# Kernel optimization log

Measured on AMD Instinct MI355X. Metric: run time of the kernel, lower is better.

## Reference

```python
import jax, jax.numpy as jnp
import numpy as np

N_SRC = 100000
N_DST = 100000
E = 500000
D = 128
L = 2


def _sage(x_src, x_dst, e_src, e_dst, W_self, W_neigh, b):
    # DGL SAGEConv('mean'): out = x_dst @ W_self^T + mean_neighbors(x_src) @ W_neigh^T + b
    n_dst = x_dst.shape[0]
    msg_sum = jax.ops.segment_sum(x_src[e_src], e_dst, num_segments=n_dst)  # [n_dst, D]
    deg = jax.ops.segment_sum(jnp.ones((e_dst.shape[0],), x_src.dtype), e_dst, num_segments=n_dst)
    h_neigh = msg_sum / jnp.maximum(deg, 1.0)[:, None]  # isolated nodes -> 0
    return x_dst @ W_self.T + h_neigh @ W_neigh.T + b


def setup_inputs() -> dict:
    key = jax.random.key(0)
    ks = jax.random.split(key, 10)
    s = 1.0 / np.sqrt(D)
    return {
        "x_src": jax.random.normal(ks[0], (N_SRC, D), jnp.float32),
        "x_dst": jax.random.normal(ks[1], (N_DST, D), jnp.float32),
        "e_src": jax.random.randint(ks[2], (E,), 0, N_SRC, jnp.int32),
        "e_dst": jax.random.randint(ks[3], (E,), 0, N_DST, jnp.int32),
        "W_ship_self": jax.random.normal(ks[4], (L, D, D), jnp.float32) * s,
        "W_ship_neigh": jax.random.normal(ks[5], (L, D, D), jnp.float32) * s,
        "b_ship": jnp.zeros((L, D), jnp.float32),
        "W_rev_self": jax.random.normal(ks[6], (L, D, D), jnp.float32) * s,
        "W_rev_neigh": jax.random.normal(ks[7], (L, D, D), jnp.float32) * s,
        "b_rev": jnp.zeros((L, D), jnp.float32),
    }


def reference(x_src, x_dst, e_src, e_dst, W_ship_self, W_ship_neigh, b_ship,
              W_rev_self, W_rev_neigh, b_rev):
    h_s, h_d = x_src, x_dst
    n_layers = W_ship_self.shape[0]
    for l in range(n_layers):
        # ('source','ship','destination'): messages source -> destination
        new_d = _sage(h_s, h_d, e_src, e_dst, W_ship_self[l], W_ship_neigh[l], b_ship[l])
        # ('destination','rev_ship','source'): messages destination -> source
        new_s = _sage(h_d, h_s, e_dst, e_src, W_rev_self[l], W_rev_neigh[l], b_rev[l])
        h_d = jax.nn.relu(new_d)
        h_s = jax.nn.relu(new_s)
        # dropout p=0.0 (eval) -> identity
    return h_s, h_d
```

## Files before the change

### kernel.cpp

```cpp
#include <hip/hip_runtime.h>
#include <hip/hip_bf16.h>

#define NN 100000
#define EDGES 500000
#define DD 128
#define NBKT 196
#define SLACK 3584
#define CHUNK 4096
#define BPD ((EDGES + CHUNK - 1) / CHUNK)

typedef short bf16x8 __attribute__((ext_vector_type(8)));
typedef float f32x4  __attribute__((ext_vector_type(4)));

__device__ __forceinline__ unsigned short f2bf(float f) {
    unsigned u = __float_as_uint(f);
    u += 0x7fffu + ((u >> 16) & 1u);
    return (unsigned short)(u >> 16);
}

__global__ void f2bx_kernel(const float* __restrict__ a, const float* __restrict__ b,
                            unsigned short* __restrict__ oa, unsigned short* __restrict__ ob) {
    const float* in = blockIdx.y ? b : a;
    unsigned short* out = blockIdx.y ? ob : oa;
    int i = blockIdx.x * 256 + threadIdx.x;
    float4 v = ((const float4*)in)[i];
    ushort4 o;
    o.x = f2bf(v.x); o.y = f2bf(v.y); o.z = f2bf(v.z); o.w = f2bf(v.w);
    ((ushort4*)out)[i] = o;
}

__global__ void f2bw_kernel(const float* __restrict__ w0, const float* __restrict__ w1,
                            const float* __restrict__ w2, const float* __restrict__ w3,
                            unsigned short* __restrict__ o0, unsigned short* __restrict__ o1,
                            unsigned short* __restrict__ o2, unsigned short* __restrict__ o3) {
    const float* in; unsigned short* out;
    switch (blockIdx.y) {
        case 0: in = w0; out = o0; break;
        case 1: in = w1; out = o1; break;
        case 2: in = w2; out = o2; break;
        default: in = w3; out = o3; break;
    }
    int i = blockIdx.x * 256 + threadIdx.x;
    float4 v = ((const float4*)in)[i];
    ushort4 o;
    o.x = f2bf(v.x); o.y = f2bf(v.y); o.z = f2bf(v.z); o.w = f2bf(v.w);
    ((ushort4*)out)[i] = o;
}

__global__ __launch_bounds__(256) void bin_scatter_kernel(
    const int* __restrict__ e_src, const int* __restrict__ e_dst,
    int* __restrict__ gcnt,
    unsigned* __restrict__ recbin)
{
    const int dir = blockIdx.y;
    const int t = threadIdx.x;
    const int c0 = blockIdx.x * CHUNK;
    const int nvalid = min(CHUNK, EDGES - c0);
    const int* __restrict__ TGT = dir ? e_src : e_dst;
    const int* __restrict__ PAY = dir ? e_dst : e_src;

    __shared__ int hist[256];
    __shared__ int lbase[256];
    __shared__ int lofs[256];
    __shared__ int scanA[256], scanB[256];
    __shared__ int laddr[CHUNK];
    __shared__ unsigned lrec[CHUNK];

    hist[t] = 0;
    __syncthreads();

    int myb[16], myslot[16];
    unsigned myrec[16];
    #pragma unroll
    for (int j = 0; j < 16; ++j) {
        int e = c0 + j * 256 + t;
        myb[j] = -1;
        if (e < EDGES) {
            int tgt = TGT[e], pay = PAY[e];
            int b = tgt >> 9;
            myb[j] = b;
            myrec[j] = ((unsigned)pay << 9) | (unsigned)(tgt & 511);
            myslot[j] = atomicAdd(&hist[b], 1);
        }
    }
    __syncthreads();
    int cnt = hist[t];
    lbase[t] = (cnt > 0) ? atomicAdd(&gcnt[dir * 256 + t], cnt) : 0;
    scanA[t] = cnt;
    __syncthreads();
    int* pa = scanA; int* pb = scanB;
    for (int d = 1; d < 256; d <<= 1) {
        pb[t] = pa[t] + (t >= d ? pa[t - d] : 0);
        __syncthreads();
        int* tmp = pa; pa = pb; pb = tmp;
    }
    lofs[t] = pa[t] - cnt;
    __syncthreads();
    #pragma unroll
    for (int j = 0; j < 16; ++j) {
        if (myb[j] >= 0) {
            int b = myb[j];
            int pos = lofs[b] + myslot[j];
            int g = lbase[b] + myslot[j];
            lrec[pos] = myrec[j];
            laddr[pos] = (g < SLACK) ? (b * SLACK + g) : -1;
        }
    }
    __syncthreads();
    unsigned* __restrict__ out = recbin + (size_t)dir * NBKT * SLACK;
    #pragma unroll
    for (int j = 0; j < 16; ++j) {
        int i = j * 256 + t;
        if (i < nvalid) {
            int a = laddr[i];
            if (a >= 0) out[a] = lrec[i];
        }
    }
}

__global__ void bucket_scan_kernel(const int* __restrict__ gcnt, int* __restrict__ csr_base) {
    int t = threadIdx.x;
    __shared__ int A[256], B[256];
    for (int dir = 0; dir < 2; ++dir) {
        int c = (t < NBKT) ? min(gcnt[dir * 256 + t], SLACK) : 0;
        A[t] = c;
        __syncthreads();
        int* pa = A; int* pb = B;
        for (int d = 1; d < 256; d <<= 1) {
            pb[t] = pa[t] + (t >= d ? pa[t - d] : 0);
            __syncthreads();
            int* tmp = pa; pa = pb; pb = tmp;
        }
        if (t < NBKT) csr_base[dir * 200 + t] = pa[t] - c;
        if (t == 0)   csr_base[dir * 200 + NBKT] = pa[255];
        __syncthreads();
    }
}

__global__ __launch_bounds__(256) void fine_place_kernel(
    const unsigned* __restrict__ recbin, const int* __restrict__ gcnt,
    const int* __restrict__ csr_base,
    int* __restrict__ rp_dst, int* __restrict__ rp_src,
    float* __restrict__ inv_dst, float* __restrict__ inv_src,
    int* __restrict__ csr_dst, int* __restrict__ csr_src)
{
    const int dir = blockIdx.y;
    const int bkt = blockIdx.x;
    const int t = threadIdx.x;
    int*   __restrict__ rp  = dir ? rp_src  : rp_dst;
    float* __restrict__ inv = dir ? inv_src : inv_dst;
    int*   __restrict__ csr = dir ? csr_src : csr_dst;
    const unsigned* __restrict__ recs = recbin + ((size_t)dir * NBKT + bkt) * SLACK;
    const int cnt = min(gcnt[dir * 256 + bkt], SLACK);
    const int cbase = csr_base[dir * 200 + bkt];
    const int n0 = bkt * 512;

    __shared__ int deg[512];
    __shared__ int sA[512], sB[512];
    __shared__ int cur[512];
    deg[t] = 0; deg[t + 256] = 0;
    __syncthreads();
    for (int i = t; i < cnt; i += 256)
        atomicAdd(&deg[recs[i] & 511u], 1);
    __syncthreads();
    sA[t] = deg[t]; sA[t + 256] = deg[t + 256];
    __syncthreads();
    int* pa = sA; int* pb = sB;
    for (int d = 1; d < 512; d <<= 1) {
        pb[t]       = pa[t]       + (t >= d           ? pa[t - d]       : 0);
        pb[t + 256] = pa[t + 256] + ((t + 256) >= d   ? pa[t + 256 - d] : 0);
        __syncthreads();
        int* tmp = pa; pa = pb; pb = tmp;
    }
    #pragma unroll
    for (int k = 0; k < 2; ++k) {
        int i = t + k * 256;
        int off = pa[i] - deg[i];
        cur[i] = off;
        int node = n0 + i;
        if (node < NN) {
            rp[node] = cbase + off;
            inv[node] = 1.0f / (float)max(deg[i], 1);
        }
    }
    if (bkt == NBKT - 1 && t == 0) rp[NN] = csr_base[dir * 200 + NBKT];
    __syncthreads();
    for (int i = t; i < cnt; i += 256) {
        unsigned r = recs[i];
        int p = atomicAdd(&cur[r & 511u], 1);
        csr[cbase + p] = (int)(r >> 9);
    }
}

__global__ void aggregate2_kernel(
    const unsigned short* __restrict__ h0, const int* __restrict__ rp0,
    const int* __restrict__ csr0, const float* __restrict__ inv0, unsigned short* __restrict__ ag0,
    const unsigned short* __restrict__ h1, const int* __restrict__ rp1,
    const int* __restrict__ csr1, const float* __restrict__ inv1, unsigned short* __restrict__ ag1)
{
    const int dir = blockIdx.y;
    const unsigned short* __restrict__ h = dir ? h1 : h0;
    const int* __restrict__ rp   = dir ? rp1 : rp0;
    const int* __restrict__ csr  = dir ? csr1 : csr0;
    const float* __restrict__ inv = dir ? inv1 : inv0;
    unsigned short* __restrict__ agg = dir ? ag1 : ag0;

    int wid  = (int)((blockIdx.x * 256u + threadIdx.x) >> 6);
    int lane = threadIdx.x & 63;
    if (wid >= NN) return;
    int beg = rp[wid], end = rp[wid + 1];
    float s0 = 0.f, s1 = 0.f, t0 = 0.f, t1 = 0.f;
    float u0 = 0.f, u1 = 0.f, v0 = 0.f, v1 = 0.f;
    int i = beg;
    for (; i + 3 < end; i += 4) {
        int c0 = csr[i], c1 = csr[i + 1], c2 = csr[i + 2], c3 = csr[i + 3];
        unsigned w0 = *(const unsigned*)(h + (size_t)c0 * DD + lane * 2);
        unsigned w1 = *(const unsigned*)(h + (size_t)c1 * DD + lane * 2);
        unsigned w2 = *(const unsigned*)(h + (size_t)c2 * DD + lane * 2);
        unsigned w3 = *(const unsigned*)(h + (size_t)c3 * DD + lane * 2);
        s0 += __uint_as_float(w0 << 16); s1 += __uint_as_float(w0 & 0xffff0000u);
        t0 += __uint_as_float(w1 << 16); t1 += __uint_as_float(w1 & 0xffff0000u);
        u0 += __uint_as_float(w2 << 16); u1 += __uint_as_float(w2 & 0xffff0000u);
        v0 += __uint_as_float(w3 << 16); v1 += __uint_as_float(w3 & 0xffff0000u);
    }
    for (; i < end; ++i) {
        unsigned w = *(const unsigned*)(h + (size_t)csr[i] * DD + lane * 2);
        s0 += __uint_as_float(w << 16); s1 += __uint_as_float(w & 0xffff0000u);
    }
    float sc = inv[wid];
    float a0 = ((s0 + t0) + (u0 + v0)) * sc;
    float a1 = ((s1 + t1) + (u1 + v1)) * sc;
    unsigned o = (unsigned)f2bf(a0) | ((unsigned)f2bf(a1) << 16);
    *(unsigned*)(agg + (size_t)wid * DD + lane * 2) = o;
}

__global__ __launch_bounds__(512, 4) void mfma_gemm5_kernel(
    const unsigned short* __restrict__ Hs0, const unsigned short* __restrict__ Ha0,
    const unsigned short* __restrict__ Ws0, const unsigned short* __restrict__ Wn0,
    const float* __restrict__ bias0, float* __restrict__ outF0, unsigned short* __restrict__ outB0,
    const unsigned short* __restrict__ Hs1, const unsigned short* __restrict__ Ha1,
    const unsigned short* __restrict__ Ws1, const unsigned short* __restrict__ Wn1,
    const float* __restrict__ bias1, float* __restrict__ outF1, unsigned short* __restrict__ outB1,
    int M)
{
    const int dir = blockIdx.y;
    const unsigned short* __restrict__ Hself = dir ? Hs1 : Hs0;
    const unsigned short* __restrict__ Hagg  = dir ? Ha1 : Ha0;
    const unsigned short* __restrict__ Wself = dir ? Ws1 : Ws0;
    const unsigned short* __restrict__ Wneigh= dir ? Wn1 : Wn0;
    const float* __restrict__ bias = dir ? bias1 : bias0;
    float* __restrict__ outF = dir ? outF1 : outF0;
    unsigned short* __restrict__ outB = dir ? outB1 : outB0;

    __shared__ __align__(16) unsigned short sW[128 * 256];
    const int tid  = threadIdx.x;
    const int lane = tid & 63;
    const int w    = tid >> 6;
    const int row0 = blockIdx.x * 256;

    #pragma unroll
    for (int i = 0; i < 8; ++i) {
        int q = i * 512 + tid;
        int n = q >> 5, c = q & 31;
        const unsigned short* src = (c < 16) ? (Wself + n * 128 + c * 8)
                                             : (Wneigh + n * 128 + (c - 16) * 8);
        int d = n * 256 + (c & 24) * 8 + (((c ^ n) & 7) * 8);
        *(uint4*)(sW + d) = *(const uint4*)src;
    }

    f32x4 acc[4][4];
    #pragma unroll
    for (int mt = 0; mt < 4; ++mt)
        #pragma unroll
        for (int nt = 0; nt < 4; ++nt) acc[mt][nt] = (f32x4){0.f, 0.f, 0.f, 0.f};

    const int mbase = (w >> 1) * 64;
    const int nbase = (w & 1) * 64;
    const int l15 = lane & 15;
    const int l4  = lane >> 4;

    int voff[4];
    #pragma unroll
    for (int mt = 0; mt < 4; ++mt) {
        int grow = row0 + mbase + mt * 16 + l15;
        if (grow >= M) grow = M - 1;
        voff[mt] = grow * 128 + l4 * 8;
    }

    __syncthreads();

    bf16x8 a_cur[4], a_nxt[4];
    #pragma unroll
    for (int mt = 0; mt < 4; ++mt) a_cur[mt] = *(const bf16x8*)(Hself + voff[mt]);

    #pragma unroll
    for (int ks = 0; ks < 8; ++ks) {
        if (ks < 7) {
            const int ks1 = ks + 1;
            const int col = (ks1 & 3) * 32;
            const unsigned short* __restrict__ base = (ks1 < 4) ? Hself : Hagg;
            #pragma unroll
            for (int mt = 0; mt < 4; ++mt)
                a_nxt[mt] = *(const bf16x8*)(base + voff[mt] + col);
        }
        const int c = ks * 4 + l4;
        #pragma unroll
        for (int mt = 0; mt < 4; ++mt) {
            int n0 = nbase + 0 * 16 + l15;
            int n1 = nbase + 1 * 16 + l15;
            int n2 = nbase + 2 * 16 + l15;
            int n3 = nbase + 3 * 16 + l15;
            bf16x8 b0 = *(const bf16x8*)(sW + n0 * 256 + (c & 24) * 8 + (((c ^ n0) & 7) * 8));
            bf16x8 b1 = *(const bf16x8*)(sW + n1 * 256 + (c & 24) * 8 + (((c ^ n1) & 7) * 8));
            bf16x8 b2 = *(const bf16x8*)(sW + n2 * 256 + (c & 24) * 8 + (((c ^ n2) & 7) * 8));
            bf16x8 b3 = *(const bf16x8*)(sW + n3 * 256 + (c & 24) * 8 + (((c ^ n3) & 7) * 8));
            acc[mt][0] = __builtin_amdgcn_mfma_f32_16x16x32_bf16(a_cur[mt], b0, acc[mt][0], 0, 0, 0);
            acc[mt][1] = __builtin_amdgcn_mfma_f32_16x16x32_bf16(a_cur[mt], b1, acc[mt][1], 0, 0, 0);
            acc[mt][2] = __builtin_amdgcn_mfma_f32_16x16x32_bf16(a_cur[mt], b2, acc[mt][2], 0, 0, 0);
            acc[mt][3] = __builtin_amdgcn_mfma_f32_16x16x32_bf16(a_cur[mt], b3, acc[mt][3], 0, 0, 0);
        }
        #pragma unroll
        for (int mt = 0; mt < 4; ++mt) a_cur[mt] = a_nxt[mt];
    }

    __syncthreads();

    #pragma unroll
    for (int nt = 0; nt < 4; ++nt) {
        int col = nbase + nt * 16 + l15;
        float bj = bias[col];
        #pragma unroll
        for (int mt = 0; mt < 4; ++mt) {
            #pragma unroll
            for (int r = 0; r < 4; ++r) {
                int grow = row0 + mbase + mt * 16 + l4 * 4 + r;
                if (grow < M) {
                    float v = fmaxf(acc[mt][nt][r] + bj, 0.f);
                    if (outF) outF[(size_t)grow * 128 + col] = v;
                    else      outB[(size_t)grow * 128 + col] = f2bf(v);
                }
            }
        }
    }
}

extern "C" void kernel_launch(void* const* d_in, const int* in_sizes, int n_in,
                              void* d_out, int out_size, void* d_ws, size_t ws_size,
                              hipStream_t stream) {
    const float* x_src        = (const float*)d_in[0];
    const float* x_dst        = (const float*)d_in[1];
    const int*   e_src        = (const int*)d_in[2];
    const int*   e_dst        = (const int*)d_in[3];
    const float* W_ship_self  = (const float*)d_in[4];
    const float* W_ship_neigh = (const float*)d_in[5];
    const float* b_ship       = (const float*)d_in[6];
    const float* W_rev_self   = (const float*)d_in[7];
    const float* W_rev_neigh  = (const float*)d_in[8];
    const float* b_rev        = (const float*)d_in[9];
    float* out = (float*)d_out;

    char* ws = (char*)d_ws;
    size_t off = 0;
    auto alloc = [&](size_t bytes) {
        char* p = ws + off;
        off = (off + bytes + 255) & ~(size_t)255;
        return p;
    };
    unsigned short* xs_bf = (unsigned short*)alloc((size_t)NN * DD * 2);
    unsigned short* xd_bf = (unsigned short*)alloc((size_t)NN * DD * 2);
    unsigned short* agg1  = (unsigned short*)alloc((size_t)NN * DD * 2);
    unsigned short* agg2  = (unsigned short*)alloc((size_t)NN * DD * 2);
    unsigned short* Wss_bf = (unsigned short*)alloc(2 * DD * DD * 2);
    unsigned short* Wsn_bf = (unsigned short*)alloc(2 * DD * DD * 2);
    unsigned short* Wrs_bf = (unsigned short*)alloc(2 * DD * DD * 2);
    unsigned short* Wrn_bf = (unsigned short*)alloc(2 * DD * DD * 2);
    int* gcnt = (int*)alloc(2 * 256 * 4);
    int* csr_base = (int*)alloc(2 * 200 * 4);
    unsigned* recbin = (unsigned*)alloc((size_t)2 * NBKT * SLACK * 4);
    int* rp_dst = (int*)alloc((NN + 1) * 4);
    int* rp_src = (int*)alloc((NN + 1) * 4);
    float* inv_dst = (float*)alloc(NN * 4);
    float* inv_src = (float*)alloc(NN * 4);
    int* csr_dst = (int*)alloc(EDGES * 4);
    int* csr_src = (int*)alloc(EDGES * 4);
    (void)ws_size; (void)in_sizes; (void)n_in; (void)out_size;

    hipMemsetAsync(gcnt, 0, 2 * 256 * 4, stream);

    const int xn4 = NN * DD / 4;
    f2bx_kernel<<<dim3(xn4 / 256, 2), 256, 0, stream>>>(x_src, x_dst, xs_bf, xd_bf);
    f2bw_kernel<<<dim3(32, 4), 256, 0, stream>>>(W_ship_self, W_ship_neigh, W_rev_self, W_rev_neigh,
                                                 Wss_bf, Wsn_bf, Wrs_bf, Wrn_bf);

    bin_scatter_kernel<<<dim3(BPD, 2), 256, 0, stream>>>(e_src, e_dst, gcnt, recbin);
    bucket_scan_kernel<<<1, 256, 0, stream>>>(gcnt, csr_base);
    fine_place_kernel<<<dim3(NBKT, 2), 256, 0, stream>>>(recbin, gcnt, csr_base,
        rp_dst, rp_src, inv_dst, inv_src, csr_dst, csr_src);

    float* out_s = out;
    float* out_d = out + (size_t)NN * DD;
    const int gemm_grid = (NN + 255) / 256;
    const int agg_grid  = (NN * 64 + 255) / 256;

    for (int l = 0; l < 2; ++l) {
        aggregate2_kernel<<<dim3(agg_grid, 2), 256, 0, stream>>>(
            xs_bf, rp_dst, csr_dst, inv_dst, agg1,
            xd_bf, rp_src, csr_src, inv_src, agg2);
        mfma_gemm5_kernel<<<dim3(gemm_grid, 2), 512, 0, stream>>>(
            xd_bf, agg1, Wss_bf + l * DD * DD, Wsn_bf + l * DD * DD, b_ship + l * DD,
            l ? out_d : nullptr, l ? nullptr : xd_bf,
            xs_bf, agg2, Wrs_bf + l * DD * DD, Wrn_bf + l * DD * DD, b_rev + l * DD,
            l ? out_s : nullptr, l ? nullptr : xs_bf,
            NN);
    }
}
```

Before: 484.5 us.

## Aggregate with 16 lanes per node using 16-byte loads and batched edge prefetch

The neighbor-mean aggregation now assigns 16 threads per destination node instead of a full 64-lane wavefront. Each thread loads 8 bf16 values with one 16-byte load, and up to 8 edges are prefetched before accumulation. The inverse degree is computed from the row pointers rather than loaded from the inv array. This is meant to cut idle lanes and raise memory-level parallelism on the random gathers, at the cost of more registers and some lane divergence for high-degree nodes.

```diff
diff --git a/kernel.cpp b/kernel.cpp
--- a/kernel.cpp
+++ b/kernel.cpp
@@ -11,6 +11,7 @@
 
 typedef short bf16x8 __attribute__((ext_vector_type(8)));
 typedef float f32x4  __attribute__((ext_vector_type(4)));
+typedef float f32x2  __attribute__((ext_vector_type(2)));
 
 __device__ __forceinline__ unsigned short f2bf(float f) {
     unsigned u = __float_as_uint(f);
@@ -192,46 +193,72 @@
     }
 }
 
-__global__ void aggregate2_kernel(
+__global__ __launch_bounds__(256) void aggregate3_kernel(
     const unsigned short* __restrict__ h0, const int* __restrict__ rp0,
-    const int* __restrict__ csr0, const float* __restrict__ inv0, unsigned short* __restrict__ ag0,
+    const int* __restrict__ csr0, unsigned short* __restrict__ ag0,
     const unsigned short* __restrict__ h1, const int* __restrict__ rp1,
-    const int* __restrict__ csr1, const float* __restrict__ inv1, unsigned short* __restrict__ ag1)
+    const int* __restrict__ csr1, unsigned short* __restrict__ ag1)
 {
     const int dir = blockIdx.y;
     const unsigned short* __restrict__ h = dir ? h1 : h0;
     const int* __restrict__ rp   = dir ? rp1 : rp0;
     const int* __restrict__ csr  = dir ? csr1 : csr0;
-    const float* __restrict__ inv = dir ? inv1 : inv0;
     unsigned short* __restrict__ agg = dir ? ag1 : ag0;
 
-    int wid  = (int)((blockIdx.x * 256u + threadIdx.x) >> 6);
-    int lane = threadIdx.x & 63;
-    if (wid >= NN) return;
-    int beg = rp[wid], end = rp[wid + 1];
-    float s0 = 0.f, s1 = 0.f, t0 = 0.f, t1 = 0.f;
-    float u0 = 0.f, u1 = 0.f, v0 = 0.f, v1 = 0.f;
-    int i = beg;
-    for (; i + 3 < end; i += 4) {
-        int c0 = csr[i], c1 = csr[i + 1], c2 = csr[i + 2], c3 = csr[i + 3];
-        unsigned w0 = *(const unsigned*)(h + (size_t)c0 * DD + lane * 2);
-        unsigned w1 = *(const unsigned*)(h + (size_t)c1 * DD + lane * 2);
-        unsigned w2 = *(const unsigned*)(h + (size_t)c2 * DD + lane * 2);
-        unsigned w3 = *(const unsigned*)(h + (size_t)c3 * DD + lane * 2);
-        s0 += __uint_as_float(w0 << 16); s1 += __uint_as_float(w0 & 0xffff0000u);
-        t0 += __uint_as_float(w1 << 16); t1 += __uint_as_float(w1 & 0xffff0000u);
-        u0 += __uint_as_float(w2 << 16); u1 += __uint_as_float(w2 & 0xffff0000u);
-        v0 += __uint_as_float(w3 << 16); v1 += __uint_as_float(w3 & 0xffff0000u);
-    }
-    for (; i < end; ++i) {
-        unsigned w = *(const unsigned*)(h + (size_t)csr[i] * DD + lane * 2);
-        s0 += __uint_as_float(w << 16); s1 += __uint_as_float(w & 0xffff0000u);
-    }
-    float sc = inv[wid];
-    float a0 = ((s0 + t0) + (u0 + v0)) * sc;
-    float a1 = ((s1 + t1) + (u1 + v1)) * sc;
-    unsigned o = (unsigned)f2bf(a0) | ((unsigned)f2bf(a1) << 16);
-    *(unsigned*)(agg + (size_t)wid * DD + lane * 2) = o;
+    const int t  = blockIdx.x * 256 + threadIdx.x;
+    const int g  = t >> 4;
+    const int sl = t & 15;
+
+    const int beg = rp[g], end = rp[g + 1];
+    const unsigned short* __restrict__ hp = h + sl * 8;
+
+    f32x2 acc[4];
+    #pragma unroll
+    for (int k = 0; k < 4; ++k) acc[k] = (f32x2){0.f, 0.f};
+
+    int cidx[8];
+    #pragma unroll
+    for (int j = 0; j < 8; ++j)
+        cidx[j] = (beg + j < end) ? csr[beg + j] : -1;
+
+    bf16x8 v[8];
+    #pragma unroll
+    for (int j = 0; j < 8; ++j)
+        if (cidx[j] >= 0)
+            v[j] = *(const bf16x8*)(hp + (size_t)cidx[j] * DD);
+
+    #pragma unroll
+    for (int j = 0; j < 8; ++j) {
+        if (cidx[j] >= 0) {
+            const unsigned* pu = (const unsigned*)&v[j];
+            #pragma unroll
+            for (int k = 0; k < 4; ++k) {
+                unsigned u = pu[k];
+                acc[k] += (f32x2){__uint_as_float(u << 16),
+                                  __uint_as_float(u & 0xffff0000u)};
+            }
+        }
+    }
+
+    for (int i = beg + 8; i < end; ++i) {
+        int c = csr[i];
+        bf16x8 w = *(const bf16x8*)(hp + (size_t)c * DD);
+        const unsigned* pu = (const unsigned*)&w;
+        #pragma unroll
+        for (int k = 0; k < 4; ++k) {
+            unsigned u = pu[k];
+            acc[k] += (f32x2){__uint_as_float(u << 16),
+                              __uint_as_float(u & 0xffff0000u)};
+        }
+    }
+
+    const float sc = 1.0f / (float)max(end - beg, 1);
+    uint4 ov;
+    ov.x = (unsigned)f2bf(acc[0].x * sc) | ((unsigned)f2bf(acc[0].y * sc) << 16);
+    ov.y = (unsigned)f2bf(acc[1].x * sc) | ((unsigned)f2bf(acc[1].y * sc) << 16);
+    ov.z = (unsigned)f2bf(acc[2].x * sc) | ((unsigned)f2bf(acc[2].y * sc) << 16);
+    ov.w = (unsigned)f2bf(acc[3].x * sc) | ((unsigned)f2bf(acc[3].y * sc) << 16);
+    *(uint4*)(agg + (size_t)g * DD + sl * 8) = ov;
 }
 
 __global__ __launch_bounds__(512, 4) void mfma_gemm5_kernel(
@@ -400,12 +427,12 @@
     float* out_s = out;
     float* out_d = out + (size_t)NN * DD;
     const int gemm_grid = (NN + 255) / 256;
-    const int agg_grid  = (NN * 64 + 255) / 256;
+    const int agg_grid  = NN * 16 / 256;
 
     for (int l = 0; l < 2; ++l) {
-        aggregate2_kernel<<<dim3(agg_grid, 2), 256, 0, stream>>>(
-            xs_bf, rp_dst, csr_dst, inv_dst, agg1,
-            xd_bf, rp_src, csr_src, inv_src, agg2);
+        aggregate3_kernel<<<dim3(agg_grid, 2), 256, 0, stream>>>(
+            xs_bf, rp_dst, csr_dst, agg1,
+            xd_bf, rp_src, csr_src, agg2);
         mfma_gemm5_kernel<<<dim3(gemm_grid, 2), 512, 0, stream>>>(
             xd_bf, agg1, Wss_bf + l * DD * DD, Wsn_bf + l * DD * DD, b_ship + l * DD,
             l ? out_d : nullptr, l ? nullptr : xd_bf,
```

Result: faster. 417.9 us (-13.8%).
